# Kernel tuning notes

Measured on AMD Instinct MI355X. Metric: run time of the kernel, lower is better.

## Reference

```python
import jax, jax.numpy as jnp
import numpy as np

NUM_NODES = 50000


def setup_inputs() -> dict:
    key = jax.random.key(0)
    ks = jax.random.split(key, 5)
    d = 128
    E = 600000
    x = jax.random.normal(ks[0], (NUM_NODES, d), dtype=jnp.float32)
    edge_attr = jax.random.normal(ks[1], (E, d), dtype=jnp.float32)
    receivers_idx = jax.random.randint(ks[2], (E,), 0, NUM_NODES)
    # MLP params: Linear(2d -> d), ReLU, Linear(d -> d). Stored as [in, out].
    W1 = jax.random.normal(ks[3], (2 * d, d), dtype=jnp.float32) / np.sqrt(2 * d)
    b1 = jnp.zeros((d,), dtype=jnp.float32)
    W2 = jax.random.normal(ks[4], (d, d), dtype=jnp.float32) / np.sqrt(d)
    b2 = jnp.zeros((d,), dtype=jnp.float32)
    return {"x": x, "edge_attr": edge_attr, "receivers_idx": receivers_idx,
            "W1": W1, "b1": b1, "W2": W2, "b2": b2}


def reference(x, edge_attr, receivers_idx, W1, b1, W2, b2):
    # scatter_add(edge_attr, receivers_idx, dim=0, dim_size=num_nodes)
    agg = jax.ops.segment_sum(edge_attr, receivers_idx, num_segments=NUM_NODES)  # [N, d]
    collected = jnp.concatenate([x, agg], axis=-1)  # [N, 2d]
    h = jax.nn.relu(collected @ W1 + b1)  # [N, d]
    out = h @ W2 + b2                     # [N, d]
    # Original returns Data(x=out, edge_attr=edge_attr, edge_index=edge_index);
    # edge_attr/edge_index pass through unchanged, so return the new node features.
    return out
```

## Files before the change

kernel.cpp:

```cpp
#include <hip/hip_runtime.h>
#include <hip/hip_bf16.h>

#define N_NODES 50000
#define DIM 128
#define N_EDGES 600000
#define MAX_DEG 64

typedef __attribute__((ext_vector_type(8))) short short8;
typedef __attribute__((ext_vector_type(4))) float f32x4;

__device__ __forceinline__ unsigned short f2bf_u(float f) {
    return __bfloat16_as_ushort(__float2bfloat16(f));
}

__global__ __launch_bounds__(256) void fill_direct(
    const int* __restrict__ ridx, int* __restrict__ cnt, int* __restrict__ elist) {
    int e = blockIdx.x * 256 + threadIdx.x;
    if (e < N_EDGES) {
        int node = ridx[e];
        int pos = atomicAdd(&cnt[node], 1);
        if (pos < MAX_DEG) elist[(size_t)node * MAX_DEG + pos] = e;
    }
}

__global__ __launch_bounds__(256) void prep_kernel(
    const float* __restrict__ W1,
    const float* __restrict__ W2,
    const float* __restrict__ x,
    __hip_bfloat16* __restrict__ W1t,
    __hip_bfloat16* __restrict__ W2t,
    __hip_bfloat16* __restrict__ xa) {
    int b = blockIdx.x;
    if (b < 192) {
        int t = b * 256 + threadIdx.x;
        if (t < 256 * 128) {
            int k = t >> 7, n = t & 127;
            W1t[n * 256 + k] = __float2bfloat16(W1[t]);
        } else {
            int q = t - 256 * 128;
            int k = q >> 7, n = q & 127;
            W2t[n * 128 + k] = __float2bfloat16(W2[q]);
        }
    } else {
        int t = (b - 192) * 256 + threadIdx.x;
        int node = t >> 5;
        int c = t & 31;
        if (node < N_NODES) {
            f32x4 v = *reinterpret_cast<const f32x4*>(x + (size_t)node * DIM + c * 4);
            ushort2 p0 = { f2bf_u(v[0]), f2bf_u(v[1]) };
            ushort2 p1 = { f2bf_u(v[2]), f2bf_u(v[3]) };
            uint2 packed = { *(unsigned*)&p0, *(unsigned*)&p1 };
            *reinterpret_cast<uint2*>(xa + (size_t)node * 256 + c * 4) = packed;
        }
    }
}

__global__ __launch_bounds__(256) void aggregate_kernel(
    const float* __restrict__ edge_attr,
    const int* __restrict__ elist,
    const int* __restrict__ cnt,
    __hip_bfloat16* __restrict__ xa) {
    const int node = blockIdx.x * 4 + (threadIdx.x >> 6);
    const int lane = threadIdx.x & 63;
    if (node >= N_NODES) return;
    int deg = cnt[node];
    deg = deg < MAX_DEG ? deg : MAX_DEG;
    const int* el = elist + (size_t)node * MAX_DEG;
    float sx = 0.f, sy = 0.f;
    int i = 0;
    for (; i + 4 <= deg; i += 4) {
        int e0 = el[i], e1 = el[i + 1], e2 = el[i + 2], e3 = el[i + 3];
        float2 v0 = *reinterpret_cast<const float2*>(edge_attr + (size_t)e0 * DIM + lane * 2);
        float2 v1 = *reinterpret_cast<const float2*>(edge_attr + (size_t)e1 * DIM + lane * 2);
        float2 v2 = *reinterpret_cast<const float2*>(edge_attr + (size_t)e2 * DIM + lane * 2);
        float2 v3 = *reinterpret_cast<const float2*>(edge_attr + (size_t)e3 * DIM + lane * 2);
        sx += (v0.x + v1.x) + (v2.x + v3.x);
        sy += (v0.y + v1.y) + (v2.y + v3.y);
    }
    for (; i < deg; i++) {
        int e0 = el[i];
        float2 v0 = *reinterpret_cast<const float2*>(edge_attr + (size_t)e0 * DIM + lane * 2);
        sx += v0.x;
        sy += v0.y;
    }
    unsigned packed = ((unsigned)f2bf_u(sy) << 16) | (unsigned)f2bf_u(sx);
    *reinterpret_cast<unsigned*>(xa + (size_t)node * 256 + 128 + lane * 2) = packed;
}

__global__ __launch_bounds__(256) void mlp_kernel(
    const __hip_bfloat16* __restrict__ xa,
    const __hip_bfloat16* __restrict__ W1t,
    const float* __restrict__ b1,
    const __hip_bfloat16* __restrict__ W2t,
    const float* __restrict__ b2,
    float* __restrict__ out) {
    __shared__ __hip_bfloat16 sH[128][136];

    const int wave = threadIdx.x >> 6;
    const int lane = threadIdx.x & 63;
    const int quad = lane >> 4;
    const int l16  = lane & 15;
    const int rowBase = blockIdx.x * 128 + wave * 32;

    f32x4 accH[2][8] = {};
#pragma unroll
    for (int ks = 0; ks < 8; ks++) {
        const int k0 = ks * 32 + quad * 8;
        short8 a[2];
#pragma unroll
        for (int rt = 0; rt < 2; rt++) {
            int row = rowBase + rt * 16 + l16;
            row = row < N_NODES ? row : N_NODES - 1;
            a[rt] = *reinterpret_cast<const short8*>(xa + (size_t)row * 256 + k0);
        }
#pragma unroll
        for (int nt = 0; nt < 8; nt++) {
            short8 b = *reinterpret_cast<const short8*>(W1t + (nt * 16 + l16) * 256 + k0);
            accH[0][nt] = __builtin_amdgcn_mfma_f32_16x16x32_bf16(a[0], b, accH[0][nt], 0, 0, 0);
            accH[1][nt] = __builtin_amdgcn_mfma_f32_16x16x32_bf16(a[1], b, accH[1][nt], 0, 0, 0);
        }
    }

#pragma unroll
    for (int nt = 0; nt < 8; nt++) {
        const float bias = b1[nt * 16 + l16];
#pragma unroll
        for (int rt = 0; rt < 2; rt++) {
#pragma unroll
            for (int i = 0; i < 4; i++) {
                float v = accH[rt][nt][i] + bias;
                v = v > 0.0f ? v : 0.0f;
                int r = wave * 32 + rt * 16 + quad * 4 + i;
                sH[r][nt * 16 + l16] = __float2bfloat16(v);
            }
        }
    }
    __syncthreads();

    f32x4 accO[2][8] = {};
#pragma unroll
    for (int ks = 0; ks < 4; ks++) {
        const int k0 = ks * 32 + quad * 8;
        short8 a[2];
#pragma unroll
        for (int rt = 0; rt < 2; rt++) {
            int r = wave * 32 + rt * 16 + l16;
            a[rt] = *reinterpret_cast<const short8*>(&sH[r][k0]);
        }
#pragma unroll
        for (int nt = 0; nt < 8; nt++) {
            short8 b = *reinterpret_cast<const short8*>(W2t + (nt * 16 + l16) * 128 + k0);
            accO[0][nt] = __builtin_amdgcn_mfma_f32_16x16x32_bf16(a[0], b, accO[0][nt], 0, 0, 0);
            accO[1][nt] = __builtin_amdgcn_mfma_f32_16x16x32_bf16(a[1], b, accO[1][nt], 0, 0, 0);
        }
    }

#pragma unroll
    for (int nt = 0; nt < 8; nt++) {
        const float bias = b2[nt * 16 + l16];
#pragma unroll
        for (int rt = 0; rt < 2; rt++) {
#pragma unroll
            for (int i = 0; i < 4; i++) {
                int row = rowBase + rt * 16 + quad * 4 + i;
                if (row < N_NODES) {
                    out[(size_t)row * DIM + nt * 16 + l16] = accO[rt][nt][i] + bias;
                }
            }
        }
    }
}

extern "C" void kernel_launch(void* const* d_in, const int* in_sizes, int n_in,
                              void* d_out, int out_size, void* d_ws, size_t ws_size,
                              hipStream_t stream) {
    const float* x         = (const float*)d_in[0];
    const float* edge_attr = (const float*)d_in[1];
    const int*   ridx      = (const int*)d_in[2];
    const float* W1        = (const float*)d_in[3];
    const float* b1        = (const float*)d_in[4];
    const float* W2        = (const float*)d_in[5];
    const float* b2        = (const float*)d_in[6];
    float* out = (float*)d_out;

    char* w = (char*)d_ws;
    int* elist = (int*)w;                     w += (size_t)N_NODES * MAX_DEG * 4;
    int* cnt   = (int*)w;                     w += (size_t)N_NODES * 4;
    __hip_bfloat16* xa  = (__hip_bfloat16*)w; w += (size_t)N_NODES * 256 * 2;
    __hip_bfloat16* W1t = (__hip_bfloat16*)w; w += 256 * 128 * 2;
    __hip_bfloat16* W2t = (__hip_bfloat16*)w;

    hipMemsetAsync(cnt, 0, (size_t)N_NODES * 4, stream);
    fill_direct<<<dim3((N_EDGES + 255) / 256), dim3(256), 0, stream>>>(ridx, cnt, elist);
    prep_kernel<<<dim3(192 + (N_NODES * 32 + 255) / 256), dim3(256), 0, stream>>>(
        W1, W2, x, W1t, W2t, xa);
    aggregate_kernel<<<dim3((N_NODES + 3) / 4), dim3(256), 0, stream>>>(edge_attr, elist, cnt, xa);
    mlp_kernel<<<dim3((N_NODES + 127) / 128), dim3(256), 0, stream>>>(xa, W1t, b1, W2t, b2, out);
}
```

Baseline: 538.6 us.

## Fuse aggregation and x conversion into MLP kernel, merge fill with weight prep

Edge aggregation now runs inside the MLP kernel: each wave gathers and sums edge features for its 32 nodes into shared memory, and x is converted to bf16 on the fly during the first GEMM. The separate aggregate and prep kernels and the intermediate xa buffer are removed, and the edge-list fill is merged with the weight transpose into one launch. This saves a global round trip of the concatenated activations and two launches. The cost is much less parallelism in the latency-bound gather: only 391 blocks, each wave walking 32 nodes in sequence, where before there was one wave per node.

```diff
diff --git a/kernel.cpp b/kernel.cpp
--- a/kernel.cpp
+++ b/kernel.cpp
@@ -5,6 +5,7 @@
 #define DIM 128
 #define N_EDGES 600000
 #define MAX_DEG 64
+#define FILL_BLOCKS ((N_EDGES + 255) / 256)
 
 typedef __attribute__((ext_vector_type(8))) short short8;
 typedef __attribute__((ext_vector_type(4))) float f32x4;
@@ -12,27 +13,22 @@
 __device__ __forceinline__ unsigned short f2bf_u(float f) {
     return __bfloat16_as_ushort(__float2bfloat16(f));
 }
+__device__ __forceinline__ short f2bf(float f) { return (short)f2bf_u(f); }
 
-__global__ __launch_bounds__(256) void fill_direct(
-    const int* __restrict__ ridx, int* __restrict__ cnt, int* __restrict__ elist) {
-    int e = blockIdx.x * 256 + threadIdx.x;
-    if (e < N_EDGES) {
-        int node = ridx[e];
-        int pos = atomicAdd(&cnt[node], 1);
-        if (pos < MAX_DEG) elist[(size_t)node * MAX_DEG + pos] = e;
-    }
-}
-
-__global__ __launch_bounds__(256) void prep_kernel(
-    const float* __restrict__ W1,
-    const float* __restrict__ W2,
-    const float* __restrict__ x,
-    __hip_bfloat16* __restrict__ W1t,
-    __hip_bfloat16* __restrict__ W2t,
-    __hip_bfloat16* __restrict__ xa) {
+__global__ __launch_bounds__(256) void fill_prep(
+    const int* __restrict__ ridx, int* __restrict__ cnt, int* __restrict__ elist,
+    const float* __restrict__ W1, const float* __restrict__ W2,
+    __hip_bfloat16* __restrict__ W1t, __hip_bfloat16* __restrict__ W2t) {
     int b = blockIdx.x;
-    if (b < 192) {
-        int t = b * 256 + threadIdx.x;
+    if (b < FILL_BLOCKS) {
+        int e = b * 256 + threadIdx.x;
+        if (e < N_EDGES) {
+            int node = ridx[e];
+            int pos = atomicAdd(&cnt[node], 1);
+            if (pos < MAX_DEG) elist[node * MAX_DEG + pos] = e;
+        }
+    } else {
+        int t = (b - FILL_BLOCKS) * 256 + threadIdx.x;
         if (t < 256 * 128) {
             int k = t >> 7, n = t & 127;
             W1t[n * 256 + k] = __float2bfloat16(W1[t]);
@@ -41,66 +37,55 @@
             int k = q >> 7, n = q & 127;
             W2t[n * 128 + k] = __float2bfloat16(W2[q]);
         }
-    } else {
-        int t = (b - 192) * 256 + threadIdx.x;
-        int node = t >> 5;
-        int c = t & 31;
-        if (node < N_NODES) {
-            f32x4 v = *reinterpret_cast<const f32x4*>(x + (size_t)node * DIM + c * 4);
-            ushort2 p0 = { f2bf_u(v[0]), f2bf_u(v[1]) };
-            ushort2 p1 = { f2bf_u(v[2]), f2bf_u(v[3]) };
-            uint2 packed = { *(unsigned*)&p0, *(unsigned*)&p1 };
-            *reinterpret_cast<uint2*>(xa + (size_t)node * 256 + c * 4) = packed;
-        }
     }
 }
 
-__global__ __launch_bounds__(256) void aggregate_kernel(
+__global__ __launch_bounds__(256) void fused_mlp(
+    const float* __restrict__ x,
     const float* __restrict__ edge_attr,
     const int* __restrict__ elist,
     const int* __restrict__ cnt,
-    __hip_bfloat16* __restrict__ xa) {
-    const int node = blockIdx.x * 4 + (threadIdx.x >> 6);
-    const int lane = threadIdx.x & 63;
-    if (node >= N_NODES) return;
-    int deg = cnt[node];
-    deg = deg < MAX_DEG ? deg : MAX_DEG;
-    const int* el = elist + (size_t)node * MAX_DEG;
-    float sx = 0.f, sy = 0.f;
-    int i = 0;
-    for (; i + 4 <= deg; i += 4) {
-        int e0 = el[i], e1 = el[i + 1], e2 = el[i + 2], e3 = el[i + 3];
-        float2 v0 = *reinterpret_cast<const float2*>(edge_attr + (size_t)e0 * DIM + lane * 2);
-        float2 v1 = *reinterpret_cast<const float2*>(edge_attr + (size_t)e1 * DIM + lane * 2);
-        float2 v2 = *reinterpret_cast<const float2*>(edge_attr + (size_t)e2 * DIM + lane * 2);
-        float2 v3 = *reinterpret_cast<const float2*>(edge_attr + (size_t)e3 * DIM + lane * 2);
-        sx += (v0.x + v1.x) + (v2.x + v3.x);
-        sy += (v0.y + v1.y) + (v2.y + v3.y);
-    }
-    for (; i < deg; i++) {
-        int e0 = el[i];
-        float2 v0 = *reinterpret_cast<const float2*>(edge_attr + (size_t)e0 * DIM + lane * 2);
-        sx += v0.x;
-        sy += v0.y;
-    }
-    unsigned packed = ((unsigned)f2bf_u(sy) << 16) | (unsigned)f2bf_u(sx);
-    *reinterpret_cast<unsigned*>(xa + (size_t)node * 256 + 128 + lane * 2) = packed;
-}
-
-__global__ __launch_bounds__(256) void mlp_kernel(
-    const __hip_bfloat16* __restrict__ xa,
     const __hip_bfloat16* __restrict__ W1t,
     const float* __restrict__ b1,
     const __hip_bfloat16* __restrict__ W2t,
     const float* __restrict__ b2,
     float* __restrict__ out) {
-    __shared__ __hip_bfloat16 sH[128][136];
+    __shared__ __hip_bfloat16 sBuf[128][136];
 
     const int wave = threadIdx.x >> 6;
     const int lane = threadIdx.x & 63;
     const int quad = lane >> 4;
     const int l16  = lane & 15;
     const int rowBase = blockIdx.x * 128 + wave * 32;
+
+    for (int n = 0; n < 32; n++) {
+        const int node = rowBase + n;
+        float sx = 0.f, sy = 0.f;
+        if (node < N_NODES) {
+            int deg = cnt[node];
+            deg = deg < MAX_DEG ? deg : MAX_DEG;
+            const int* el = elist + node * MAX_DEG;
+            int i = 0;
+            for (; i + 4 <= deg; i += 4) {
+                int e0 = el[i], e1 = el[i + 1], e2 = el[i + 2], e3 = el[i + 3];
+                float2 v0 = *reinterpret_cast<const float2*>(edge_attr + (size_t)e0 * DIM + lane * 2);
+                float2 v1 = *reinterpret_cast<const float2*>(edge_attr + (size_t)e1 * DIM + lane * 2);
+                float2 v2 = *reinterpret_cast<const float2*>(edge_attr + (size_t)e2 * DIM + lane * 2);
+                float2 v3 = *reinterpret_cast<const float2*>(edge_attr + (size_t)e3 * DIM + lane * 2);
+                sx += (v0.x + v1.x) + (v2.x + v3.x);
+                sy += (v0.y + v1.y) + (v2.y + v3.y);
+            }
+            for (; i < deg; i++) {
+                int e0 = el[i];
+                float2 v0 = *reinterpret_cast<const float2*>(edge_attr + (size_t)e0 * DIM + lane * 2);
+                sx += v0.x;
+                sy += v0.y;
+            }
+        }
+        unsigned packed = ((unsigned)f2bf_u(sy) << 16) | (unsigned)f2bf_u(sx);
+        *reinterpret_cast<unsigned*>(&sBuf[wave * 32 + n][lane * 2]) = packed;
+    }
+    __syncthreads();
 
     f32x4 accH[2][8] = {};
 #pragma unroll
@@ -109,9 +94,20 @@
         short8 a[2];
 #pragma unroll
         for (int rt = 0; rt < 2; rt++) {
-            int row = rowBase + rt * 16 + l16;
-            row = row < N_NODES ? row : N_NODES - 1;
-            a[rt] = *reinterpret_cast<const short8*>(xa + (size_t)row * 256 + k0);
+            if (ks < 4) {
+                int row = rowBase + rt * 16 + l16;
+                row = row < N_NODES ? row : N_NODES - 1;
+                const float* p = x + (size_t)row * DIM + k0;
+                f32x4 f0 = *reinterpret_cast<const f32x4*>(p);
+                f32x4 f1 = *reinterpret_cast<const f32x4*>(p + 4);
+                short8 s;
+#pragma unroll
+                for (int i = 0; i < 4; i++) { s[i] = f2bf(f0[i]); s[4 + i] = f2bf(f1[i]); }
+                a[rt] = s;
+            } else {
+                int r = wave * 32 + rt * 16 + l16;
+                a[rt] = *reinterpret_cast<const short8*>(&sBuf[r][k0 - 128]);
+            }
         }
 #pragma unroll
         for (int nt = 0; nt < 8; nt++) {
@@ -120,6 +116,7 @@
             accH[1][nt] = __builtin_amdgcn_mfma_f32_16x16x32_bf16(a[1], b, accH[1][nt], 0, 0, 0);
         }
     }
+    __syncthreads();
 
 #pragma unroll
     for (int nt = 0; nt < 8; nt++) {
@@ -131,7 +128,7 @@
                 float v = accH[rt][nt][i] + bias;
                 v = v > 0.0f ? v : 0.0f;
                 int r = wave * 32 + rt * 16 + quad * 4 + i;
-                sH[r][nt * 16 + l16] = __float2bfloat16(v);
+                sBuf[r][nt * 16 + l16] = __float2bfloat16(v);
             }
         }
     }
@@ -145,7 +142,7 @@
 #pragma unroll
         for (int rt = 0; rt < 2; rt++) {
             int r = wave * 32 + rt * 16 + l16;
-            a[rt] = *reinterpret_cast<const short8*>(&sH[r][k0]);
+            a[rt] = *reinterpret_cast<const short8*>(&sBuf[r][k0]);
         }
 #pragma unroll
         for (int nt = 0; nt < 8; nt++) {
@@ -186,14 +183,12 @@
     char* w = (char*)d_ws;
     int* elist = (int*)w;                     w += (size_t)N_NODES * MAX_DEG * 4;
     int* cnt   = (int*)w;                     w += (size_t)N_NODES * 4;
-    __hip_bfloat16* xa  = (__hip_bfloat16*)w; w += (size_t)N_NODES * 256 * 2;
     __hip_bfloat16* W1t = (__hip_bfloat16*)w; w += 256 * 128 * 2;
     __hip_bfloat16* W2t = (__hip_bfloat16*)w;
 
     hipMemsetAsync(cnt, 0, (size_t)N_NODES * 4, stream);
-    fill_direct<<<dim3((N_EDGES + 255) / 256), dim3(256), 0, stream>>>(ridx, cnt, elist);
-    prep_kernel<<<dim3(192 + (N_NODES * 32 + 255) / 256), dim3(256), 0, stream>>>(
-        W1, W2, x, W1t, W2t, xa);
-    aggregate_kernel<<<dim3((N_NODES + 3) / 4), dim3(256), 0, stream>>>(edge_attr, elist, cnt, xa);
-    mlp_kernel<<<dim3((N_NODES + 127) / 128), dim3(256), 0, stream>>>(xa, W1t, b1, W2t, b2, out);
+    fill_prep<<<dim3(FILL_BLOCKS + 192), dim3(256), 0, stream>>>(
+        ridx, cnt, elist, W1, W2, W1t, W2t);
+    fused_mlp<<<dim3((N_NODES + 127) / 128), dim3(256), 0, stream>>>(
+        x, edge_attr, elist, cnt, W1t, b1, W2t, b2, out);
 }
```

Result: slower. 599.2 us (+11.2%).
